# Optimization experiments

Measured on AMD Instinct MI355X. Metric: run time of the kernel, lower is better.

Reference implementation:

```python
import jax, jax.numpy as jnp
import numpy as np

N_USERS = 30000
N_ENT = 70000
N = N_USERS + N_ENT          # total graph nodes
E = 1_600_000                # edges (avg degree 16)
D = 64                       # embed_dim
B = 4096                     # scored user-item pairs
LEAKY_SLOPE = 0.01           # torch nn.LeakyReLU default
EPS = 1e-12                  # torch F.normalize default eps


def setup_inputs() -> dict:
    key = jax.random.key(0)
    ks = jax.random.split(key, 16)
    inp = {
        "edge_row": jax.random.randint(ks[0], (E,), 0, N, dtype=jnp.int32),
        "edge_col": jax.random.randint(ks[1], (E,), 0, N, dtype=jnp.int32),
        "edge_vals": jax.random.uniform(ks[2], (E,), dtype=jnp.float32) / 16.0,
        "user_embed": jax.random.normal(ks[3], (N_USERS, D), jnp.float32) * 0.1,
        "entity_embed": jax.random.normal(ks[4], (N_ENT, D), jnp.float32) * 0.1,
        "W1_0": jax.random.normal(ks[5], (D, 64), jnp.float32) * (1.0 / np.sqrt(D)),
        "b1_0": jnp.zeros((64,), jnp.float32),
        "W2_0": jax.random.normal(ks[6], (D, 64), jnp.float32) * (1.0 / np.sqrt(D)),
        "b2_0": jnp.zeros((64,), jnp.float32),
        "W1_1": jax.random.normal(ks[7], (64, 32), jnp.float32) * (1.0 / 8.0),
        "b1_1": jnp.zeros((32,), jnp.float32),
        "W2_1": jax.random.normal(ks[8], (64, 32), jnp.float32) * (1.0 / 8.0),
        "b2_1": jnp.zeros((32,), jnp.float32),
        "user_ids": jax.random.randint(ks[9], (B,), 0, N_USERS, dtype=jnp.int32),
        "item_ids": jax.random.randint(ks[10], (B,), 0, N_ENT, dtype=jnp.int32),
    }
    return inp


def _gnn_layer(feats, edge_row, edge_col, edge_vals, W1, b1, W2, b2):
    # sparse adj @ feats  ==  scatter-add of weighted source features to rows
    gathered = feats[edge_col] * edge_vals[:, None]          # (E, d_in)
    h_neigh = jax.ops.segment_sum(gathered, edge_row, num_segments=N)  # (N, d_in)
    term1 = (feats + h_neigh) @ W1 + b1
    term2 = (feats * h_neigh) @ W2 + b2
    h = jax.nn.leaky_relu(term1 + term2, negative_slope=LEAKY_SLOPE)
    # F.normalize(h, p=2, dim=1)
    norm = jnp.linalg.norm(h, axis=1, keepdims=True)
    return h / jnp.maximum(norm, EPS)


def reference(edge_row, edge_col, edge_vals, user_embed, entity_embed,
              W1_0, b1_0, W2_0, b2_0, W1_1, b1_1, W2_1, b2_1,
              user_ids, item_ids):
    a0 = jnp.concatenate([user_embed, entity_embed], axis=0)     # (N, 64)
    a1 = _gnn_layer(a0, edge_row, edge_col, edge_vals, W1_0, b1_0, W2_0, b2_0)  # (N, 64)
    a2 = _gnn_layer(a1, edge_row, edge_col, edge_vals, W1_1, b1_1, W2_1, b2_1)  # (N, 32)
    final = jnp.concatenate([a0, a1, a2], axis=1)                # (N, 160)
    u = final[user_ids]                                          # (B, 160)
    i = final[N_USERS + item_ids]                                # (B, 160)
    return jnp.sum(u * i, axis=1)                                # (B,)
```

## Files before the change

kernel.cpp:

```cpp
#include <hip/hip_runtime.h>
#include <hip/hip_bf16.h>
#include <math.h>

#define LEAKY 0.01f
#define SCAN_BLOCK 256
#define SCAN_ITEMS 4
#define SCAN_TILE (SCAN_BLOCK * SCAN_ITEMS)

struct __align__(8) Bf4 { __hip_bfloat16 a, b, c, d; };

__global__ void count_edges(const int* __restrict__ row, int E,
                            int* __restrict__ deg, int* __restrict__ rank) {
    int i = blockIdx.x * blockDim.x + threadIdx.x;
    if (i < E) rank[i] = atomicAdd(&deg[row[i]], 1);
}

__global__ __launch_bounds__(SCAN_BLOCK) void scan_phase1(
    const int* __restrict__ deg, int* __restrict__ blocksum, int N) {
    __shared__ int red[SCAN_BLOCK];
    int b = blockIdx.x, t = threadIdx.x;
    int base = b * SCAN_TILE + t * SCAN_ITEMS;
    int s = 0;
#pragma unroll
    for (int j = 0; j < SCAN_ITEMS; j++) {
        int i = base + j;
        if (i < N) s += deg[i];
    }
    red[t] = s;
    __syncthreads();
    for (int off = SCAN_BLOCK / 2; off > 0; off >>= 1) {
        if (t < off) red[t] += red[t + off];
        __syncthreads();
    }
    if (t == 0) blocksum[b] = red[0];
}

__global__ __launch_bounds__(1024) void scan_phase2(
    const int* __restrict__ blocksum, int* __restrict__ blockoff,
    int* __restrict__ row_ptr, int G, int N) {
    __shared__ int sums[1024];
    int t = threadIdx.x;
    sums[t] = (t < G) ? blocksum[t] : 0;
    __syncthreads();
    for (int off = 1; off < 1024; off <<= 1) {
        int v = (t >= off) ? sums[t - off] : 0;
        __syncthreads();
        sums[t] += v;
        __syncthreads();
    }
    if (t < G) blockoff[t] = (t == 0) ? 0 : sums[t - 1];
    if (t == G - 1) row_ptr[N] = sums[t];
}

__global__ __launch_bounds__(SCAN_BLOCK) void scan_phase3(
    const int* __restrict__ deg, const int* __restrict__ blockoff,
    int* __restrict__ row_ptr, int N) {
    __shared__ int red[SCAN_BLOCK];
    int b = blockIdx.x, t = threadIdx.x;
    int base = b * SCAN_TILE + t * SCAN_ITEMS;
    int v[SCAN_ITEMS];
    int s = 0;
#pragma unroll
    for (int j = 0; j < SCAN_ITEMS; j++) {
        int i = base + j;
        v[j] = (i < N) ? deg[i] : 0;
        s += v[j];
    }
    red[t] = s;
    __syncthreads();
    for (int off = 1; off < SCAN_BLOCK; off <<= 1) {
        int x = (t >= off) ? red[t - off] : 0;
        __syncthreads();
        red[t] += x;
        __syncthreads();
    }
    int run = blockoff[b] + ((t == 0) ? 0 : red[t - 1]);
#pragma unroll
    for (int j = 0; j < SCAN_ITEMS; j++) {
        int i = base + j;
        if (i < N) { row_ptr[i] = run; run += v[j]; }
    }
}

__global__ void build_a0b(const float4* __restrict__ ue, const float4* __restrict__ ee,
                          __hip_bfloat16* __restrict__ a0b, int nu4, int ntot4) {
    int i = blockIdx.x * blockDim.x + threadIdx.x;
    if (i < ntot4) {
        float4 v = (i < nu4) ? ue[i] : ee[i - nu4];
        Bf4 q = {__float2bfloat16(v.x), __float2bfloat16(v.y),
                 __float2bfloat16(v.z), __float2bfloat16(v.w)};
        *(Bf4*)&a0b[(size_t)i * 4] = q;
    }
}

__global__ void fill_csr(const int* __restrict__ row, const int* __restrict__ col,
                         const float* __restrict__ val, const int* __restrict__ rank,
                         const int* __restrict__ row_ptr, int E,
                         int2* __restrict__ csr) {
    int i = blockIdx.x * blockDim.x + threadIdx.x;
    if (i < E) {
        int p = row_ptr[row[i]] + rank[i];
        csr[p] = make_int2(col[i], __float_as_int(val[i]));
    }
}

__device__ __forceinline__ void fma4(float o[4], float sv, const float4& wv) {
    o[0] = fmaf(sv, wv.x, o[0]);
    o[1] = fmaf(sv, wv.y, o[1]);
    o[2] = fmaf(sv, wv.z, o[2]);
    o[3] = fmaf(sv, wv.w, o[3]);
}

template<int DOUT>
__global__ __launch_bounds__(256, 8) void gnn_layer(
    const float* __restrict__ featsU, const float* __restrict__ featsE, int NUo,
    const __hip_bfloat16* __restrict__ featsb,
    const int2* __restrict__ csr, const int* __restrict__ row_ptr,
    const float* __restrict__ W1, const float* __restrict__ b1,
    const float* __restrict__ W2, const float* __restrict__ b2,
    float* __restrict__ out, __hip_bfloat16* __restrict__ outb, int N) {
    __shared__ __align__(16) float S[32 * 132];
    int wv = threadIdx.x >> 6, lane = threadIdx.x & 63;
    int nb = blockIdx.x * 32 + wv * 8;
    int sl = lane & 31;
    int selbase = lane & 32;

    int rp_l = row_ptr[min(nb + min(lane, 8), N)];
    int e0[8], dg[8];
#pragma unroll
    for (int ni = 0; ni < 8; ni++) {
        int a = __builtin_amdgcn_readlane(rp_l, ni);
        int b = __builtin_amdgcn_readlane(rp_l, ni + 1);
        e0[ni] = a; dg[ni] = b - a;
    }

    const uint* fb2 = (const uint*)featsb;
    const float2* f2u = (const float2*)featsU;
    const float2* f2e = (const float2*)featsE;

    int2 m0[4];
    float2 xv[4];
#pragma unroll
    for (int pr = 0; pr < 4; pr++) {
        int idx = 2 * pr + (selbase ? 1 : 0);
        int myDg = dg[idx], myE0 = e0[idx];
        m0[pr] = make_int2(0, 0);
        if (sl < min(myDg, 32)) m0[pr] = csr[myE0 + sl];
        int nn = min(nb + idx, N - 1);
        xv[pr] = (nn < NUo) ? f2u[(size_t)nn * 32 + sl]
                            : f2e[(size_t)(nn - NUo) * 32 + sl];
    }

#pragma unroll
    for (int pr = 0; pr < 4; pr++) {
        int idx = 2 * pr + (selbase ? 1 : 0);
        int myDg = dg[idx], myE0 = e0[idx];
        int mx = max(dg[2 * pr], dg[2 * pr + 1]);
        float accx = 0.f, accy = 0.f;
        int lim = min(mx, 32);
        for (int c = 0; c < lim; c += 8) {
            uint w[8]; float vv[8];
#pragma unroll
            for (int u = 0; u < 8; u++) {
                int j = c + u;
                int col = __shfl(m0[pr].x, selbase + j, 64);
                vv[u] = __int_as_float(__shfl(m0[pr].y, selbase + j, 64));
                w[u] = fb2[(size_t)col * 32 + sl];
            }
#pragma unroll
            for (int u = 0; u < 8; u++) {
                accx = fmaf(vv[u], __uint_as_float(w[u] << 16), accx);
                accy = fmaf(vv[u], __uint_as_float(w[u] & 0xffff0000u), accy);
            }
        }
        if (mx > 32) {
            for (int done = 32; done < mx; done += 32) {
                int2 mt = make_int2(0, 0);
                if (sl < myDg - done) mt = csr[myE0 + done + sl];
                int lim2 = min(mx - done, 32);
                for (int c = 0; c < lim2; c += 8) {
                    uint w[8]; float vv[8];
#pragma unroll
                    for (int u = 0; u < 8; u++) {
                        int j = c + u;
                        int col = __shfl(mt.x, selbase + j, 64);
                        vv[u] = __int_as_float(__shfl(mt.y, selbase + j, 64));
                        w[u] = fb2[(size_t)col * 32 + sl];
                    }
#pragma unroll
                    for (int u = 0; u < 8; u++) {
                        accx = fmaf(vv[u], __uint_as_float(w[u] << 16), accx);
                        accy = fmaf(vv[u], __uint_as_float(w[u] & 0xffff0000u), accy);
                    }
                }
            }
        }
        if (nb + idx < N) {
            float* sp = &S[(wv * 8 + idx) * 132];
            *(float2*)&sp[2 * sl]      = make_float2(xv[pr].x + accx, xv[pr].y + accy);
            *(float2*)&sp[64 + 2 * sl] = make_float2(xv[pr].x * accx, xv[pr].y * accy);
        }
    }
    __threadfence_block();

    if constexpr (DOUT == 64) {
        int strip = lane & 15, g = lane >> 4;
        int d0 = strip * 4;
        float4 b1v = *(const float4*)&b1[d0];
        float4 b2v = *(const float4*)&b2[d0];
        float oa[4] = {b1v.x + b2v.x, b1v.y + b2v.y, b1v.z + b2v.z, b1v.w + b2v.w};
        float ob[4] = {oa[0], oa[1], oa[2], oa[3]};
        const float* spa = &S[(wv * 8 + 2 * g) * 132];
        const float* spb = spa + 132;
#pragma unroll
        for (int half = 0; half < 2; half++) {
            const float* W  = half ? W2 : W1;
            const float* sa = spa + half * 64;
            const float* sb = spb + half * 64;
#pragma unroll 2
            for (int k = 0; k < 64; k += 4) {
                float4 va = *(const float4*)&sa[k];
                float4 vb = *(const float4*)&sb[k];
                float4 wr0 = *(const float4*)&W[(k + 0) * 64 + d0];
                float4 wr1 = *(const float4*)&W[(k + 1) * 64 + d0];
                float4 wr2 = *(const float4*)&W[(k + 2) * 64 + d0];
                float4 wr3 = *(const float4*)&W[(k + 3) * 64 + d0];
                fma4(oa, va.x, wr0); fma4(oa, va.y, wr1);
                fma4(oa, va.z, wr2); fma4(oa, va.w, wr3);
                fma4(ob, vb.x, wr0); fma4(ob, vb.y, wr1);
                fma4(ob, vb.z, wr2); fma4(ob, vb.w, wr3);
            }
        }
#pragma unroll
        for (int t = 0; t < 2; t++) {
            float* o = t ? ob : oa;
            float h0 = (o[0] > 0.f) ? o[0] : LEAKY * o[0];
            float h1 = (o[1] > 0.f) ? o[1] : LEAKY * o[1];
            float h2 = (o[2] > 0.f) ? o[2] : LEAKY * o[2];
            float h3 = (o[3] > 0.f) ? o[3] : LEAKY * o[3];
            float ss = h0 * h0 + h1 * h1 + h2 * h2 + h3 * h3;
            ss += __shfl_xor(ss, 1, 64);
            ss += __shfl_xor(ss, 2, 64);
            ss += __shfl_xor(ss, 4, 64);
            ss += __shfl_xor(ss, 8, 64);
            float sc = 1.0f / fmaxf(sqrtf(ss), 1e-12f);
            int node = nb + 2 * g + t;
            if (node < N) {
                float4 r = {h0 * sc, h1 * sc, h2 * sc, h3 * sc};
                *(float4*)&out[(size_t)node * 64 + d0] = r;
                Bf4 q = {__float2bfloat16(r.x), __float2bfloat16(r.y),
                         __float2bfloat16(r.z), __float2bfloat16(r.w)};
                *(Bf4*)&outb[(size_t)node * 64 + d0] = q;
            }
        }
    } else {
        int strip = lane & 7, nI = lane >> 3;
        int d0 = strip * 4;
        float4 b1v = *(const float4*)&b1[d0];
        float4 b2v = *(const float4*)&b2[d0];
        float o[4] = {b1v.x + b2v.x, b1v.y + b2v.y, b1v.z + b2v.z, b1v.w + b2v.w};
        const float* sp = &S[(wv * 8 + nI) * 132];
#pragma unroll
        for (int half = 0; half < 2; half++) {
            const float* W  = half ? W2 : W1;
            const float* sv = sp + half * 64;
#pragma unroll 2
            for (int k = 0; k < 64; k += 4) {
                float4 v   = *(const float4*)&sv[k];
                float4 wr0 = *(const float4*)&W[(k + 0) * 32 + d0];
                float4 wr1 = *(const float4*)&W[(k + 1) * 32 + d0];
                float4 wr2 = *(const float4*)&W[(k + 2) * 32 + d0];
                float4 wr3 = *(const float4*)&W[(k + 3) * 32 + d0];
                fma4(o, v.x, wr0); fma4(o, v.y, wr1);
                fma4(o, v.z, wr2); fma4(o, v.w, wr3);
            }
        }
        float h0 = (o[0] > 0.f) ? o[0] : LEAKY * o[0];
        float h1 = (o[1] > 0.f) ? o[1] : LEAKY * o[1];
        float h2 = (o[2] > 0.f) ? o[2] : LEAKY * o[2];
        float h3 = (o[3] > 0.f) ? o[3] : LEAKY * o[3];
        float ss = h0 * h0 + h1 * h1 + h2 * h2 + h3 * h3;
        ss += __shfl_xor(ss, 1, 64);
        ss += __shfl_xor(ss, 2, 64);
        ss += __shfl_xor(ss, 4, 64);
        float sc = 1.0f / fmaxf(sqrtf(ss), 1e-12f);
        int node = nb + nI;
        if (node < N) {
            float4 r = {h0 * sc, h1 * sc, h2 * sc, h3 * sc};
            *(float4*)&out[(size_t)node * 32 + d0] = r;
        }
    }
}

__global__ __launch_bounds__(256) void score_pairs(
    const float* __restrict__ ue, const float* __restrict__ ee,
    const float* __restrict__ a1, const float* __restrict__ a2,
    const int* __restrict__ uid, const int* __restrict__ iid,
    float* __restrict__ out, int B, int NU) {
    int wave = threadIdx.x >> 6, lane = threadIdx.x & 63;
    int p = blockIdx.x * 4 + wave;
    if (p >= B) return;
    int u = uid[p], it = iid[p];
    size_t un = (size_t)u, in = (size_t)(NU + it);
    float s = ue[un * 64 + lane] * ee[(size_t)it * 64 + lane];
    s = fmaf(a1[un * 64 + lane], a1[in * 64 + lane], s);
    if (lane < 32) s = fmaf(a2[un * 32 + lane], a2[in * 32 + lane], s);
#pragma unroll
    for (int m = 32; m >= 1; m >>= 1) s += __shfl_xor(s, m, 64);
    if (lane == 0) out[p] = s;
}

extern "C" void kernel_launch(void* const* d_in, const int* in_sizes, int n_in,
                              void* d_out, int out_size, void* d_ws, size_t ws_size,
                              hipStream_t stream) {
    const int*   edge_row  = (const int*)d_in[0];
    const int*   edge_col  = (const int*)d_in[1];
    const float* edge_vals = (const float*)d_in[2];
    const float* ue        = (const float*)d_in[3];
    const float* ee        = (const float*)d_in[4];
    const float* W1_0 = (const float*)d_in[5];
    const float* b1_0 = (const float*)d_in[6];
    const float* W2_0 = (const float*)d_in[7];
    const float* b2_0 = (const float*)d_in[8];
    const float* W1_1 = (const float*)d_in[9];
    const float* b1_1 = (const float*)d_in[10];
    const float* W2_1 = (const float*)d_in[11];
    const float* b2_1 = (const float*)d_in[12];
    const int*   uid  = (const int*)d_in[13];
    const int*   iid  = (const int*)d_in[14];
    float* out = (float*)d_out;

    const int E  = in_sizes[0];
    const int NU = in_sizes[3] / 64;
    const int NE = in_sizes[4] / 64;
    const int N  = NU + NE;
    const int B  = in_sizes[13];
    const int G  = (N + SCAN_TILE - 1) / SCAN_TILE;

    char* ws = (char*)d_ws;
    size_t off = 0;
    auto alloc = [&](size_t bytes) -> char* {
        char* p = ws + off;
        off = (off + bytes + 255) & ~(size_t)255;
        return p;
    };
    int*   deg      = (int*)alloc((size_t)N * 4);
    int*   rank     = (int*)alloc((size_t)E * 4);
    int*   row_ptr  = (int*)alloc((size_t)(N + 1) * 4);
    int*   blocksum = (int*)alloc((size_t)1024 * 4);
    int*   blockoff = (int*)alloc((size_t)1024 * 4);
    int2*  csr      = (int2*)alloc((size_t)E * 8);
    float* a1       = (float*)alloc((size_t)N * 64 * 4);
    float* a2       = (float*)alloc((size_t)N * 32 * 4);
    __hip_bfloat16* a0b = (__hip_bfloat16*)alloc((size_t)N * 64 * 2);
    __hip_bfloat16* a1b = (__hip_bfloat16*)alloc((size_t)N * 64 * 2);
    (void)ws_size; (void)n_in; (void)out_size; (void)NE;

    hipMemsetAsync(deg, 0, (size_t)N * 4, stream);
    count_edges<<<(E + 255) / 256, 256, 0, stream>>>(edge_row, E, deg, rank);
    scan_phase1<<<G, SCAN_BLOCK, 0, stream>>>(deg, blocksum, N);
    scan_phase2<<<1, 1024, 0, stream>>>(blocksum, blockoff, row_ptr, G, N);
    scan_phase3<<<G, SCAN_BLOCK, 0, stream>>>(deg, blockoff, row_ptr, N);
    fill_csr<<<(E + 255) / 256, 256, 0, stream>>>(edge_row, edge_col, edge_vals,
                                                  rank, row_ptr, E, csr);
    int ntot4 = N * 16, nu4 = NU * 16;
    build_a0b<<<(ntot4 + 255) / 256, 256, 0, stream>>>((const float4*)ue, (const float4*)ee,
                                                       a0b, nu4, ntot4);
    gnn_layer<64><<<(N + 31) / 32, 256, 0, stream>>>(ue, ee, NU, a0b, csr, row_ptr,
                                                     W1_0, b1_0, W2_0, b2_0, a1, a1b, N);
    gnn_layer<32><<<(N + 31) / 32, 256, 0, stream>>>(a1, a1, N, a1b, csr, row_ptr,
                                                     W1_1, b1_1, W2_1, b2_1, a2, nullptr, N);
    score_pairs<<<(B + 3) / 4, 256, 0, stream>>>(ue, ee, a1, a2, uid, iid, out, B, NU);
}
```

Before: 379.2 us.

## Fuse CSR prep kernels and replace rank array with decrementing atomics

Merges edge counting with the bf16 conversion of the initial embeddings into one kernel, and folds the single-block scan phase into the per-block scan by having each block sum the preceding block totals itself. The per-edge rank array is removed: fill_csr now claims slots by atomically decrementing the degree counters. This cuts two kernel launches and the rank array's write and read traffic, but adds a second pass of contended atomics, makes the order of edges within each row nondeterministic, and has each scan block redundantly read up to G block sums.

```diff
diff --git a/kernel.cpp b/kernel.cpp
--- a/kernel.cpp
+++ b/kernel.cpp
@@ -9,10 +9,18 @@
 
 struct __align__(8) Bf4 { __hip_bfloat16 a, b, c, d; };
 
-__global__ void count_edges(const int* __restrict__ row, int E,
-                            int* __restrict__ deg, int* __restrict__ rank) {
+__global__ void prep(const int* __restrict__ row, int E,
+                     int* __restrict__ deg,
+                     const float4* __restrict__ ue, const float4* __restrict__ ee,
+                     __hip_bfloat16* __restrict__ a0b, int nu4, int ntot4) {
     int i = blockIdx.x * blockDim.x + threadIdx.x;
-    if (i < E) rank[i] = atomicAdd(&deg[row[i]], 1);
+    if (i < E) atomicAdd(&deg[row[i]], 1);
+    if (i < ntot4) {
+        float4 v = (i < nu4) ? ue[i] : ee[i - nu4];
+        Bf4 q = {__float2bfloat16(v.x), __float2bfloat16(v.y),
+                 __float2bfloat16(v.z), __float2bfloat16(v.w)};
+        *(Bf4*)&a0b[(size_t)i * 4] = q;
+    }
 }
 
 __global__ __launch_bounds__(SCAN_BLOCK) void scan_phase1(
@@ -35,28 +43,22 @@
     if (t == 0) blocksum[b] = red[0];
 }
 
-__global__ __launch_bounds__(1024) void scan_phase2(
-    const int* __restrict__ blocksum, int* __restrict__ blockoff,
-    int* __restrict__ row_ptr, int G, int N) {
-    __shared__ int sums[1024];
-    int t = threadIdx.x;
-    sums[t] = (t < G) ? blocksum[t] : 0;
-    __syncthreads();
-    for (int off = 1; off < 1024; off <<= 1) {
-        int v = (t >= off) ? sums[t - off] : 0;
-        __syncthreads();
-        sums[t] += v;
-        __syncthreads();
-    }
-    if (t < G) blockoff[t] = (t == 0) ? 0 : sums[t - 1];
-    if (t == G - 1) row_ptr[N] = sums[t];
-}
-
-__global__ __launch_bounds__(SCAN_BLOCK) void scan_phase3(
-    const int* __restrict__ deg, const int* __restrict__ blockoff,
+__global__ __launch_bounds__(SCAN_BLOCK) void scan_phase23(
+    const int* __restrict__ deg, const int* __restrict__ blocksum,
     int* __restrict__ row_ptr, int N) {
     __shared__ int red[SCAN_BLOCK];
+    __shared__ int boff_s;
     int b = blockIdx.x, t = threadIdx.x;
+    int part = 0;
+    for (int j = t; j < b; j += SCAN_BLOCK) part += blocksum[j];
+    red[t] = part;
+    __syncthreads();
+    for (int off = SCAN_BLOCK / 2; off > 0; off >>= 1) {
+        if (t < off) red[t] += red[t + off];
+        __syncthreads();
+    }
+    if (t == 0) boff_s = red[0];
+    __syncthreads();
     int base = b * SCAN_TILE + t * SCAN_ITEMS;
     int v[SCAN_ITEMS];
     int s = 0;
@@ -74,33 +76,27 @@
         red[t] += x;
         __syncthreads();
     }
-    int run = blockoff[b] + ((t == 0) ? 0 : red[t - 1]);
+    int run = boff_s + ((t == 0) ? 0 : red[t - 1]);
 #pragma unroll
     for (int j = 0; j < SCAN_ITEMS; j++) {
         int i = base + j;
-        if (i < N) { row_ptr[i] = run; run += v[j]; }
-    }
-}
-
-__global__ void build_a0b(const float4* __restrict__ ue, const float4* __restrict__ ee,
-                          __hip_bfloat16* __restrict__ a0b, int nu4, int ntot4) {
-    int i = blockIdx.x * blockDim.x + threadIdx.x;
-    if (i < ntot4) {
-        float4 v = (i < nu4) ? ue[i] : ee[i - nu4];
-        Bf4 q = {__float2bfloat16(v.x), __float2bfloat16(v.y),
-                 __float2bfloat16(v.z), __float2bfloat16(v.w)};
-        *(Bf4*)&a0b[(size_t)i * 4] = q;
+        if (i < N) {
+            row_ptr[i] = run;
+            run += v[j];
+            if (i == N - 1) row_ptr[N] = run;
+        }
     }
 }
 
 __global__ void fill_csr(const int* __restrict__ row, const int* __restrict__ col,
-                         const float* __restrict__ val, const int* __restrict__ rank,
-                         const int* __restrict__ row_ptr, int E,
-                         int2* __restrict__ csr) {
+                         const float* __restrict__ val,
+                         int* __restrict__ deg, const int* __restrict__ row_ptr,
+                         int E, int2* __restrict__ csr) {
     int i = blockIdx.x * blockDim.x + threadIdx.x;
     if (i < E) {
-        int p = row_ptr[row[i]] + rank[i];
-        csr[p] = make_int2(col[i], __float_as_int(val[i]));
+        int r = row[i];
+        int c = atomicAdd(&deg[r], -1);
+        csr[row_ptr[r] + c - 1] = make_int2(col[i], __float_as_int(val[i]));
     }
 }
 
@@ -345,10 +341,8 @@
         return p;
     };
     int*   deg      = (int*)alloc((size_t)N * 4);
-    int*   rank     = (int*)alloc((size_t)E * 4);
     int*   row_ptr  = (int*)alloc((size_t)(N + 1) * 4);
     int*   blocksum = (int*)alloc((size_t)1024 * 4);
-    int*   blockoff = (int*)alloc((size_t)1024 * 4);
     int2*  csr      = (int2*)alloc((size_t)E * 8);
     float* a1       = (float*)alloc((size_t)N * 64 * 4);
     float* a2       = (float*)alloc((size_t)N * 32 * 4);
@@ -356,16 +350,17 @@
     __hip_bfloat16* a1b = (__hip_bfloat16*)alloc((size_t)N * 64 * 2);
     (void)ws_size; (void)n_in; (void)out_size; (void)NE;
 
+    int ntot4 = N * 16, nu4 = NU * 16;
+    int prepN = max(E, ntot4);
+
     hipMemsetAsync(deg, 0, (size_t)N * 4, stream);
-    count_edges<<<(E + 255) / 256, 256, 0, stream>>>(edge_row, E, deg, rank);
+    prep<<<(prepN + 255) / 256, 256, 0, stream>>>(edge_row, E, deg,
+                                                  (const float4*)ue, (const float4*)ee,
+                                                  a0b, nu4, ntot4);
     scan_phase1<<<G, SCAN_BLOCK, 0, stream>>>(deg, blocksum, N);
-    scan_phase2<<<1, 1024, 0, stream>>>(blocksum, blockoff, row_ptr, G, N);
-    scan_phase3<<<G, SCAN_BLOCK, 0, stream>>>(deg, blockoff, row_ptr, N);
+    scan_phase23<<<G, SCAN_BLOCK, 0, stream>>>(deg, blocksum, row_ptr, N);
     fill_csr<<<(E + 255) / 256, 256, 0, stream>>>(edge_row, edge_col, edge_vals,
-                                                  rank, row_ptr, E, csr);
-    int ntot4 = N * 16, nu4 = NU * 16;
-    build_a0b<<<(ntot4 + 255) / 256, 256, 0, stream>>>((const float4*)ue, (const float4*)ee,
-                                                       a0b, nu4, ntot4);
+                                                  deg, row_ptr, E, csr);
     gnn_layer<64><<<(N + 31) / 32, 256, 0, stream>>>(ue, ee, NU, a0b, csr, row_ptr,
                                                      W1_0, b1_0, W2_0, b2_0, a1, a1b, N);
     gnn_layer<32><<<(N + 31) / 32, 256, 0, stream>>>(a1, a1, N, a1b, csr, row_ptr,
```

Result: slower. 415.8 us (+9.6%).
